# Kernel optimization log

Measured on AMD Instinct MI355X. Metric: run time of the kernel, lower is better.

The kernel has to match this reference:

```python
import jax, jax.numpy as jnp
import numpy as np

N, B, H, L0, L1, C = 196608, 4096, 230, 10, 53, 53


def setup_inputs() -> dict:
    key = jax.random.key(0)
    ks = jax.random.split(key, 12)
    x = jax.random.normal(ks[0], (N, H), jnp.float32)
    label_index = jax.random.randint(ks[1], (N,), 0, C, dtype=jnp.int32)
    rl0 = jax.random.randint(ks[2], (C, 1), 0, L0, dtype=jnp.int32)
    rl1 = jax.random.randint(ks[3], (C, 1), 0, L1, dtype=jnp.int32)
    relation_levels = jnp.concatenate([rl0, rl1], axis=1)  # [C, 2]
    # equal-size bags: 4096 bags of 48 sentences (ragged boundaries)
    scope = (jnp.arange(B + 1, dtype=jnp.int32) * (N // B))
    rel_emb0 = jax.random.normal(ks[4], (L0, H), jnp.float32)
    rel_emb1 = jax.random.normal(ks[5], (L1, H), jnp.float32)
    att_w0 = jax.random.normal(ks[6], (L0,), jnp.float32)
    att_w1 = jax.random.normal(ks[7], (L1,), jnp.float32)
    w_s = jax.random.normal(ks[8], (2, 3 * H), jnp.float32) * 0.05
    b_s = jax.random.normal(ks[9], (2, 1), jnp.float32) * 0.05
    disc_matrix = jax.random.normal(ks[10], (C, 2 * H), jnp.float32) * 0.05
    bias = jnp.zeros((C,), jnp.float32)
    return {"x": x, "rel_emb0": rel_emb0, "rel_emb1": rel_emb1,
            "att_w0": att_w0, "att_w1": att_w1, "w_s": w_s, "b_s": b_s,
            "disc_matrix": disc_matrix, "bias": bias,
            "label_index": label_index, "relation_levels": relation_levels,
            "scope": scope}


def _segment_softmax(logits, seg, num_seg):
    # logits: [N]; stable softmax within each bag (segment)
    m = jax.ops.segment_max(logits, seg, num_segments=num_seg)
    e = jnp.exp(logits - m[seg])
    z = jax.ops.segment_sum(e, seg, num_segments=num_seg)
    return e / z[seg]


def reference(x, rel_emb0, rel_emb1, att_w0, att_w1, w_s, b_s, disc_matrix,
              bias, label_index, relation_levels, scope):
    n, h = x.shape
    num_bags = scope.shape[0] - 1
    # bag id of each sentence from ragged boundaries
    seg = jnp.searchsorted(scope, jnp.arange(n, dtype=scope.dtype), side="right") - 1

    ll = relation_levels[label_index]                 # [N, 2]
    r0 = rel_emb0[ll[:, 0]]                           # [N, H]
    r1 = rel_emb1[ll[:, 1]]                           # [N, H]
    s = jnp.tanh(jnp.concatenate([x, r0, r1], axis=-1))  # [N, 3H]
    logits = w_s @ s.T + b_s                          # [2, N]

    # per-bag ragged softmax over sentences, per hierarchy level
    score = jax.vmap(lambda l: _segment_softmax(l, seg, num_bags))(logits)  # [2, N]

    # vertical (hierarchy) attention: softmax over hier per sentence, mean per bag
    v = jnp.stack([att_w0[ll[:, 0]], att_w1[ll[:, 1]]])  # [2, N]
    vsm = jax.nn.softmax(v, axis=0)                      # [2, N]
    counts = jax.ops.segment_sum(jnp.ones((n,), x.dtype), seg, num_segments=num_bags)
    layer_att = jax.vmap(lambda r: jax.ops.segment_sum(r, seg, num_segments=num_bags))(vsm) / counts  # [2, B]

    # attention-weighted bag representation: per bag, [2, len] @ [len, H]
    rep = jax.vmap(lambda sc: jax.ops.segment_sum(sc[:, None] * x, seg, num_segments=num_bags))(score)  # [2, B, H]
    tower = (layer_att[:, :, None] * rep).transpose(1, 0, 2).reshape(num_bags, 2 * h)  # [B, 2H]

    return tower @ disc_matrix.T + bias  # [B, C]
```

## Files before the change

kernel.cpp:

```cpp
#include <hip/hip_runtime.h>

#define NTOT 196608
#define BAGS 4096
#define H 230
#define H3 690
#define NC 53

__device__ __forceinline__ float fast_tanh(float x) {
    float e = __expf(2.f * x);
    float r = __builtin_amdgcn_rcpf(e + 1.f);
    return fmaf(-2.f, r, 1.f);
}

__global__ void class_table_kernel(const float* __restrict__ rel_emb0,
                                   const float* __restrict__ rel_emb1,
                                   const float* __restrict__ att_w0,
                                   const float* __restrict__ att_w1,
                                   const float* __restrict__ w_s,
                                   const float* __restrict__ b_s,
                                   const int* __restrict__ relation_levels,
                                   float* __restrict__ cls)
{
    int c = blockIdx.x;
    int lane = threadIdx.x;
    int l0 = relation_levels[c * 2 + 0];
    int l1 = relation_levels[c * 2 + 1];
    float a00 = 0.f, a01 = 0.f, a10 = 0.f, a11 = 0.f;
    for (int j = lane; j < H; j += 64) {
        float t0 = fast_tanh(rel_emb0[l0 * H + j]);
        float t1 = fast_tanh(rel_emb1[l1 * H + j]);
        a00 += w_s[0 * H3 + H + j] * t0;
        a01 += w_s[0 * H3 + 2 * H + j] * t1;
        a10 += w_s[1 * H3 + H + j] * t0;
        a11 += w_s[1 * H3 + 2 * H + j] * t1;
    }
    for (int m = 32; m; m >>= 1) {
        a00 += __shfl_xor(a00, m);
        a01 += __shfl_xor(a01, m);
        a10 += __shfl_xor(a10, m);
        a11 += __shfl_xor(a11, m);
    }
    if (lane == 0) {
        cls[0 * NC + c] = a00 + a01 + b_s[0];
        cls[1 * NC + c] = a10 + a11 + b_s[1];
        float v0 = att_w0[l0], v1 = att_w1[l1];
        float mx = fmaxf(v0, v1);
        float e0 = __expf(v0 - mx), e1 = __expf(v1 - mx);
        float rz = __builtin_amdgcn_rcpf(e0 + e1);
        cls[2 * NC + c] = e0 * rz;
        cls[3 * NC + c] = e1 * rz;
    }
}

__global__ __launch_bounds__(256, 8) void bag_kernel(
    const float* __restrict__ x,
    const float* __restrict__ w_s,
    const float* __restrict__ disc,
    const float* __restrict__ bias,
    const int* __restrict__ label_index,
    const int* __restrict__ scope,
    const float* __restrict__ cls,
    float* __restrict__ out)
{
    __shared__ __align__(16) float part[4][464];
    __shared__ float zs[4][4];
    __shared__ __align__(16) float t01[464];

    int b = blockIdx.x;
    int start = scope[b];
    int cnt = scope[b + 1] - start;
    int tid = threadIdx.x;
    int wave = tid >> 6;
    int lane = tid & 63;
    const float* xb = x + (long long)start * H;

    float w0r[4], w1r[4];
#pragma unroll
    for (int u = 0; u < 4; ++u) {
        int jj = lane + 64 * u;
        w0r[u] = (jj < H) ? w_s[jj] : 0.f;
        w1r[u] = (jj < H) ? w_s[H3 + jj] : 0.f;
    }

    float acc0[4] = {0.f, 0.f, 0.f, 0.f};
    float acc1[4] = {0.f, 0.f, 0.f, 0.f};
    float z0 = 0.f, z1 = 0.f, sv0 = 0.f, sv1 = 0.f;

    for (int t = 0; t < 12; ++t) {
        int i = wave + 4 * t;
        if (i >= cnt) break;
        const float* row = xb + i * H;
        float r[4];
        float d0 = 0.f, d1 = 0.f;
#pragma unroll
        for (int u = 0; u < 4; ++u) {
            int jj = lane + 64 * u;
            r[u] = (jj < H) ? row[jj] : 0.f;
        }
#pragma unroll
        for (int u = 0; u < 4; ++u) {
            float tnh = fast_tanh(r[u]);
            d0 += w0r[u] * tnh;
            d1 += w1r[u] * tnh;
        }
#pragma unroll
        for (int m = 32; m; m >>= 1) {
            d0 += __shfl_xor(d0, m);
            d1 += __shfl_xor(d1, m);
        }
        int c = label_index[start + i];
        float e0 = __expf(d0 + cls[c]);
        float e1 = __expf(d1 + cls[NC + c]);
        z0 += e0; z1 += e1;
        sv0 += cls[2 * NC + c];
        sv1 += cls[3 * NC + c];
#pragma unroll
        for (int u = 0; u < 4; ++u) {
            acc0[u] = fmaf(e0, r[u], acc0[u]);
            acc1[u] = fmaf(e1, r[u], acc1[u]);
        }
    }

#pragma unroll
    for (int u = 0; u < 4; ++u) {
        int jj = lane + 64 * u;
        if (jj < H) {
            part[wave][jj]     = acc0[u];
            part[wave][H + jj] = acc1[u];
        }
    }
    if (lane == 0) {
        zs[wave][0] = z0; zs[wave][1] = z1;
        zs[wave][2] = sv0; zs[wave][3] = sv1;
    }
    __syncthreads();

    float zt0 = zs[0][0] + zs[1][0] + zs[2][0] + zs[3][0];
    float zt1 = zs[0][1] + zs[1][1] + zs[2][1] + zs[3][1];
    float st0 = zs[0][2] + zs[1][2] + zs[2][2] + zs[3][2];
    float st1 = zs[0][3] + zs[1][3] + zs[2][3] + zs[3][3];
    float rc  = __builtin_amdgcn_rcpf((float)cnt);
    float s0  = st0 * rc * __builtin_amdgcn_rcpf(zt0);
    float s1  = st1 * rc * __builtin_amdgcn_rcpf(zt1);

    for (int t = tid; t < 2 * H; t += 256) {
        float s = part[0][t] + part[1][t] + part[2][t] + part[3][t];
        t01[t] = s * (t < H ? s0 : s1);
    }
    __syncthreads();

    int q = tid & 3;
    int c = tid >> 2;
    if (c < NC) {
        const float4* drow4 = (const float4*)(disc + c * (2 * H));
        const float4* t4 = (const float4*)t01;
        float acc = 0.f;
        for (int k = q; k < 115; k += 4) {
            float4 dv = drow4[k];
            float4 tv = t4[k];
            acc += dv.x * tv.x + dv.y * tv.y + dv.z * tv.z + dv.w * tv.w;
        }
        acc += __shfl_down(acc, 2, 4);
        acc += __shfl_down(acc, 1, 4);
        if (q == 0) out[b * NC + c] = acc + bias[c];
    }
}

extern "C" void kernel_launch(void* const* d_in, const int* in_sizes, int n_in,
                              void* d_out, int out_size, void* d_ws, size_t ws_size,
                              hipStream_t stream) {
    const float* x               = (const float*)d_in[0];
    const float* rel_emb0        = (const float*)d_in[1];
    const float* rel_emb1        = (const float*)d_in[2];
    const float* att_w0          = (const float*)d_in[3];
    const float* att_w1          = (const float*)d_in[4];
    const float* w_s             = (const float*)d_in[5];
    const float* b_s             = (const float*)d_in[6];
    const float* disc            = (const float*)d_in[7];
    const float* bias            = (const float*)d_in[8];
    const int*   label_index     = (const int*)d_in[9];
    const int*   relation_levels = (const int*)d_in[10];
    const int*   scope           = (const int*)d_in[11];
    float* out = (float*)d_out;
    float* cls = (float*)d_ws;

    class_table_kernel<<<NC, 64, 0, stream>>>(rel_emb0, rel_emb1, att_w0, att_w1,
                                              w_s, b_s, relation_levels, cls);
    bag_kernel<<<BAGS, 256, 0, stream>>>(x, w_s, disc, bias, label_index, scope,
                                         cls, out);
}
```

Measured before the change: 301.0 us.

## Preload all bag rows as float2 into registers and batch reductions

Each wave now issues all 12 of its row loads up front as float2 vector loads into registers. It then computes the tanh dot products for every row and performs the shuffle reductions interleaved across all rows, instead of running a serial load-reduce-accumulate loop per row. The aim is more memory-level parallelism and fewer dependent shuffle chains on the bandwidth-bound read of x. In exchange, register pressure rises sharply, so the launch-bounds occupancy hint is lowered from 8 to 4 blocks per CU.

```diff
diff --git a/kernel.cpp b/kernel.cpp
--- a/kernel.cpp
+++ b/kernel.cpp
@@ -5,6 +5,7 @@
 #define H 230
 #define H3 690
 #define NC 53
+#define NP 115
 
 __device__ __forceinline__ float fast_tanh(float x) {
     float e = __expf(2.f * x);
@@ -52,7 +53,7 @@
     }
 }
 
-__global__ __launch_bounds__(256, 8) void bag_kernel(
+__global__ __launch_bounds__(256, 4) void bag_kernel(
     const float* __restrict__ x,
     const float* __restrict__ w_s,
     const float* __restrict__ disc,
@@ -74,59 +75,87 @@
     int lane = tid & 63;
     const float* xb = x + (long long)start * H;
 
-    float w0r[4], w1r[4];
-#pragma unroll
-    for (int u = 0; u < 4; ++u) {
-        int jj = lane + 64 * u;
-        w0r[u] = (jj < H) ? w_s[jj] : 0.f;
-        w1r[u] = (jj < H) ? w_s[H3 + jj] : 0.f;
-    }
-
-    float acc0[4] = {0.f, 0.f, 0.f, 0.f};
-    float acc1[4] = {0.f, 0.f, 0.f, 0.f};
+    const float2* w0p = (const float2*)w_s;
+    const float2* w1p = (const float2*)(w_s + H3);
+    float2 w0r[2], w1r[2];
+#pragma unroll
+    for (int u = 0; u < 2; ++u) {
+        int p = lane + 64 * u;
+        if (p < NP) { w0r[u] = w0p[p]; w1r[u] = w1p[p]; }
+        else        { w0r[u] = make_float2(0.f, 0.f); w1r[u] = make_float2(0.f, 0.f); }
+    }
+
+    float2 r[12][2];
+#pragma unroll
+    for (int k = 0; k < 12; ++k) {
+        int i = wave + 4 * k;
+        int ic = (i < cnt) ? i : 0;
+        const float2* row2 = (const float2*)(xb + ic * H);
+#pragma unroll
+        for (int u = 0; u < 2; ++u) {
+            int p = lane + 64 * u;
+            r[k][u] = (p < NP) ? row2[p] : make_float2(0.f, 0.f);
+        }
+    }
+
+    float d0[12], d1[12];
+#pragma unroll
+    for (int k = 0; k < 12; ++k) {
+        float a0 = 0.f, a1 = 0.f;
+#pragma unroll
+        for (int u = 0; u < 2; ++u) {
+            float tx = fast_tanh(r[k][u].x);
+            float ty = fast_tanh(r[k][u].y);
+            a0 += w0r[u].x * tx + w0r[u].y * ty;
+            a1 += w1r[u].x * tx + w1r[u].y * ty;
+        }
+        d0[k] = a0; d1[k] = a1;
+    }
+
+#pragma unroll
+    for (int m = 32; m; m >>= 1) {
+#pragma unroll
+        for (int k = 0; k < 12; ++k) {
+            d0[k] += __shfl_xor(d0[k], m);
+            d1[k] += __shfl_xor(d1[k], m);
+        }
+    }
+
+    float2 acc0[2], acc1[2];
+#pragma unroll
+    for (int u = 0; u < 2; ++u) {
+        acc0[u] = make_float2(0.f, 0.f);
+        acc1[u] = make_float2(0.f, 0.f);
+    }
     float z0 = 0.f, z1 = 0.f, sv0 = 0.f, sv1 = 0.f;
-
-    for (int t = 0; t < 12; ++t) {
-        int i = wave + 4 * t;
-        if (i >= cnt) break;
-        const float* row = xb + i * H;
-        float r[4];
-        float d0 = 0.f, d1 = 0.f;
-#pragma unroll
-        for (int u = 0; u < 4; ++u) {
-            int jj = lane + 64 * u;
-            r[u] = (jj < H) ? row[jj] : 0.f;
-        }
-#pragma unroll
-        for (int u = 0; u < 4; ++u) {
-            float tnh = fast_tanh(r[u]);
-            d0 += w0r[u] * tnh;
-            d1 += w1r[u] * tnh;
-        }
-#pragma unroll
-        for (int m = 32; m; m >>= 1) {
-            d0 += __shfl_xor(d0, m);
-            d1 += __shfl_xor(d1, m);
-        }
-        int c = label_index[start + i];
-        float e0 = __expf(d0 + cls[c]);
-        float e1 = __expf(d1 + cls[NC + c]);
+#pragma unroll
+    for (int k = 0; k < 12; ++k) {
+        int i = wave + 4 * k;
+        bool act = (i < cnt);
+        int ic = act ? i : 0;
+        int c = label_index[start + ic];
+        float e0 = act ? __expf(d0[k] + cls[c])      : 0.f;
+        float e1 = act ? __expf(d1[k] + cls[NC + c]) : 0.f;
         z0 += e0; z1 += e1;
-        sv0 += cls[2 * NC + c];
-        sv1 += cls[3 * NC + c];
-#pragma unroll
-        for (int u = 0; u < 4; ++u) {
-            acc0[u] = fmaf(e0, r[u], acc0[u]);
-            acc1[u] = fmaf(e1, r[u], acc1[u]);
-        }
-    }
-
-#pragma unroll
-    for (int u = 0; u < 4; ++u) {
-        int jj = lane + 64 * u;
-        if (jj < H) {
-            part[wave][jj]     = acc0[u];
-            part[wave][H + jj] = acc1[u];
+        sv0 += act ? cls[2 * NC + c] : 0.f;
+        sv1 += act ? cls[3 * NC + c] : 0.f;
+#pragma unroll
+        for (int u = 0; u < 2; ++u) {
+            acc0[u].x = fmaf(e0, r[k][u].x, acc0[u].x);
+            acc0[u].y = fmaf(e0, r[k][u].y, acc0[u].y);
+            acc1[u].x = fmaf(e1, r[k][u].x, acc1[u].x);
+            acc1[u].y = fmaf(e1, r[k][u].y, acc1[u].y);
+        }
+    }
+
+#pragma unroll
+    for (int u = 0; u < 2; ++u) {
+        int p = lane + 64 * u;
+        if (p < NP) {
+            part[wave][2 * p]         = acc0[u].x;
+            part[wave][2 * p + 1]     = acc0[u].y;
+            part[wave][H + 2 * p]     = acc1[u].x;
+            part[wave][H + 2 * p + 1] = acc1[u].y;
         }
     }
     if (lane == 0) {
```

After: 346.7 us. +15.2%, slower.
